# Performance work log

Measured on AMD Instinct MI355X. Metric: run time of the kernel, lower is better.

The kernel has to match this reference:

```python
import jax, jax.numpy as jnp
import numpy as np

EPS = 1e-06


def setup_inputs() -> dict:
    key = jax.random.key(0)
    k1, k2, k3 = jax.random.split(key, 3)
    B, L, S, C = 128, 512, 512, 64
    q = jax.random.normal(k1, (B, L, C), dtype=jnp.float32)
    k = jax.random.normal(k2, (B, S, C), dtype=jnp.float32)
    labels = jax.random.randint(k3, (B, L, S), 0, 2, dtype=jnp.int64)
    return {"q": q, "k": k, "labels": labels}


def reference(q, k, labels):
    # sim: [B, L, S], mapped to (0, 1) via (1 + cos-like sim) / 2
    sim = (1.0 + jnp.einsum('blc,bsc->bls', q, k)) * 0.5

    # column-wise stats (over L) -> [B, S]; torch.std uses ddof=1 (unbiased)
    col = (jnp.max(sim, axis=1) - jnp.mean(sim, axis=1)) / jnp.std(sim, axis=1, ddof=1)
    sharp1 = jax.nn.softmax(col, axis=-1)  # [B, S]

    # row-wise stats (over S) -> [B, L]
    row = (jnp.max(sim, axis=2) - jnp.mean(sim, axis=2)) / jnp.std(sim, axis=2, ddof=1)
    sharp2 = jax.nn.softmax(row, axis=-1)  # [B, L]

    simc = jnp.clip(sim, EPS, 1.0 - EPS)
    nll = -jnp.log(simc)                    # [B, L, S]
    nll_neg = -jnp.log(1.0 - simc)          # [B, L, S]

    pos = (labels == 1).astype(sim.dtype)
    neg = (labels == 0).astype(sim.dtype)

    # masked sums per sample, weighted by sharpness (broadcast over rows/cols)
    loss1 = jnp.sum(nll * sharp1[:, None, :] * pos, axis=(1, 2))  # [B]
    loss2 = jnp.sum(nll * sharp2[:, :, None] * pos, axis=(1, 2))  # [B]
    loss3 = jnp.sum(nll_neg * neg, axis=(1, 2)) / jnp.sum(neg, axis=(1, 2))  # [B]

    losses = (loss1 + loss2) * 0.5 + loss3
    return (sharp1, jnp.mean(losses))
```

## Files before the change

### kernel.cpp

```cpp
#include <hip/hip_runtime.h>

#define EPSF 1e-6f

typedef _Float16 half8 __attribute__((ext_vector_type(8)));
typedef float f32x4 __attribute__((ext_vector_type(4)));

constexpr int B = 128, L = 512, S = 512, C = 64;
constexpr int TILE_R = 64;
constexpr int TILES  = L / TILE_R;
constexpr int CHUNK  = 64;
constexpr int NCHUNK = S / CHUNK;
constexpr int HALVES = 2;
constexpr int CPB    = NCHUNK / HALVES;

constexpr size_t WS_COLMAX = 0;
constexpr size_t WS_COLSUM = WS_COLMAX + (size_t)B * TILES * S;
constexpr size_t WS_COLSSQ = WS_COLSUM + (size_t)B * TILES * S;
constexpr size_t WS_COLP1  = WS_COLSSQ + (size_t)B * TILES * S;
constexpr size_t WS_ROWMAX = WS_COLP1  + (size_t)B * TILES * S;
constexpr size_t WS_ROWSUM = WS_ROWMAX + (size_t)B * L * HALVES;
constexpr size_t WS_ROWSSQ = WS_ROWSUM + (size_t)B * L * HALVES;
constexpr size_t WS_ROWP2  = WS_ROWSSQ + (size_t)B * L * HALVES;
constexpr size_t WS_NEGS   = WS_ROWP2  + (size_t)B * L * HALVES;
constexpr size_t WS_NEGC   = WS_NEGS   + (size_t)B * TILES * HALVES;

__device__ inline void loadTile(const float* __restrict__ g, float4 v[4], int t)
{
    const float* src = g + (t >> 2) * 64 + (t & 3) * 16;
    v[0] = *(const float4*)(src);
    v[1] = *(const float4*)(src + 4);
    v[2] = *(const float4*)(src + 8);
    v[3] = *(const float4*)(src + 12);
}

__device__ inline void stageW(const float4 v4[4], half8 (*hiA)[64], half8 (*loA)[64], int t)
{
    const int row = t >> 2, c0 = (t & 3) * 16;
    const float v[16] = {v4[0].x, v4[0].y, v4[0].z, v4[0].w, v4[1].x, v4[1].y, v4[1].z, v4[1].w,
                         v4[2].x, v4[2].y, v4[2].z, v4[2].w, v4[3].x, v4[3].y, v4[3].z, v4[3].w};
#pragma unroll
    for (int o = 0; o < 2; ++o) {
        const int cb     = c0 + o * 8;
        const int idx    = (row >> 4) * 2 + (cb >> 5);
        const int lane_s = (((cb >> 3) & 3) << 4) + (row & 15);
        half8 h, l;
#pragma unroll
        for (int j = 0; j < 8; ++j) {
            float f = v[o * 8 + j];
            _Float16 hi = (_Float16)f;
            h[j] = hi;
            l[j] = (_Float16)(f - (float)hi);
        }
        hiA[idx][lane_s] = h;
        loA[idx][lane_s] = l;
    }
}

__global__ __launch_bounds__(256) __attribute__((amdgpu_waves_per_eu(3, 8)))
void pass1_kernel(const float* __restrict__ q, const float* __restrict__ kmat,
                  const int* __restrict__ labels, float* __restrict__ ws)
{
    __shared__ half8 khiF[8][64], kloF[8][64];
    __shared__ float4 colred4[4][CHUNK];
    __shared__ float nred[4][2];

    const int bidx = blockIdx.x;
    const int b    = bidx / (TILES * HALVES);
    const int rem  = bidx % (TILES * HALVES);
    const int tile = rem >> 1;
    const int half = rem & 1;
    const int chbase = half * CPB;
    const int tid  = threadIdx.x;
    const int lane = tid & 63;
    const int wave = tid >> 6;
    const int l15  = lane & 15;
    const int quad = lane >> 4;
    const int rowbase = tile * TILE_R;

    float* colmax_p = ws + WS_COLMAX;
    float* colsum_p = ws + WS_COLSUM;
    float* colssq_p = ws + WS_COLSSQ;
    float* colp1_p  = ws + WS_COLP1;
    float* rowmax_p = ws + WS_ROWMAX;
    float* rowsum_p = ws + WS_ROWSUM;
    float* rowssq_p = ws + WS_ROWSSQ;
    float* rowp2_p  = ws + WS_ROWP2;
    float* negs_p   = ws + WS_NEGS;
    float* negc_p   = ws + WS_NEGC;

    const float* kb = kmat + (size_t)b * S * C;
    const int*   lb = labels + ((size_t)b * L + rowbase) * S;

    float4 tv[4];
    loadTile(q + ((size_t)b * L + rowbase) * C, tv, tid);
    stageW(tv, khiF, kloF, tid);
    int labn[16];
#pragma unroll
    for (int ct = 0; ct < 4; ++ct)
#pragma unroll
        for (int r = 0; r < 4; ++r)
            labn[ct * 4 + r] = lb[(size_t)(wave * 16 + quad * 4 + r) * S
                                  + chbase * CHUNK + ct * 16 + l15];
    __syncthreads();
    half8 ah0 = khiF[wave * 2 + 0][lane], ah1 = khiF[wave * 2 + 1][lane];
    half8 al0 = kloF[wave * 2 + 0][lane], al1 = kloF[wave * 2 + 1][lane];
    loadTile(kb + (size_t)chbase * CHUNK * C, tv, tid);

    float rmax[4], rsum[4], rssq[4], rp2[4];
#pragma unroll
    for (int i = 0; i < 4; ++i) { rmax[i] = -3.4e38f; rsum[i] = 0.f; rssq[i] = 0.f; rp2[i] = 0.f; }
    float negsum = 0.f;
    int   possum = 0;

    for (int c4 = 0; c4 < CPB; ++c4) {
        const int ch = chbase + c4;
        __syncthreads();
        if (c4 > 0 && tid < CHUNK) {
            float4 v = colred4[0][tid];
            float m0 = v.x, s1 = v.y, s2 = v.z, pp = v.w;
#pragma unroll
            for (int w = 1; w < 4; ++w) {
                float4 u = colred4[w][tid];
                m0 = fmaxf(m0, u.x); s1 += u.y; s2 += u.z; pp += u.w;
            }
            size_t idx = ((size_t)b * TILES + tile) * S + (ch - 1) * CHUNK + tid;
            colmax_p[idx] = m0; colsum_p[idx] = s1; colssq_p[idx] = s2; colp1_p[idx] = pp;
        }
        stageW(tv, khiF, kloF, tid);
        if (c4 + 1 < CPB)
            loadTile(kb + (size_t)(ch + 1) * CHUNK * C, tv, tid);
        __syncthreads();

        f32x4 acc[4];
#pragma unroll
        for (int ct = 0; ct < 4; ++ct) {
            half8 bh0 = khiF[ct * 2 + 0][lane], bh1 = khiF[ct * 2 + 1][lane];
            half8 bl0 = kloF[ct * 2 + 0][lane], bl1 = kloF[ct * 2 + 1][lane];
            f32x4 a = {0.f, 0.f, 0.f, 0.f};
            a = __builtin_amdgcn_mfma_f32_16x16x32_f16(ah0, bh0, a, 0, 0, 0);
            a = __builtin_amdgcn_mfma_f32_16x16x32_f16(ah0, bl0, a, 0, 0, 0);
            a = __builtin_amdgcn_mfma_f32_16x16x32_f16(al0, bh0, a, 0, 0, 0);
            a = __builtin_amdgcn_mfma_f32_16x16x32_f16(ah1, bh1, a, 0, 0, 0);
            a = __builtin_amdgcn_mfma_f32_16x16x32_f16(ah1, bl1, a, 0, 0, 0);
            a = __builtin_amdgcn_mfma_f32_16x16x32_f16(al1, bh1, a, 0, 0, 0);
            acc[ct] = a;
        }

#pragma unroll
        for (int ct = 0; ct < 4; ++ct) {
            float cmax = -3.4e38f, csum = 0.f, cssq = 0.f, cp1 = 0.f;
#pragma unroll
            for (int r = 0; r < 4; ++r) {
                int lab = labn[ct * 4 + r];
                float sim = fmaf(0.5f, acc[ct][r], 0.5f);
                rmax[r] = fmaxf(rmax[r], sim);
                rsum[r] += sim;
                rssq[r] = fmaf(sim, sim, rssq[r]);
                cmax = fmaxf(cmax, sim);
                csum += sim;
                cssq = fmaf(sim, sim, cssq);
                float sc  = fminf(fmaxf(sim, EPSF), 1.f - EPSF);
                bool  isp = (lab == 1);
                float pos = isp ? 1.f : 0.f;
                float t   = isp ? sc : (1.f - sc);
                float nl  = -__logf(t);
                float pn  = pos * nl;
                rp2[r] += pn;
                cp1 += pn;
                negsum += nl - pn;
                possum += lab;
            }
#pragma unroll
            for (int m = 16; m <= 32; m <<= 1) {
                cmax = fmaxf(cmax, __shfl_xor(cmax, m, 64));
                csum += __shfl_xor(csum, m, 64);
                cssq += __shfl_xor(cssq, m, 64);
                cp1  += __shfl_xor(cp1,  m, 64);
            }
            if (lane < 16)
                colred4[wave][ct * 16 + l15] = make_float4(cmax, csum, cssq, cp1);
        }

        if (c4 + 1 < CPB) {
#pragma unroll
            for (int ct = 0; ct < 4; ++ct)
#pragma unroll
                for (int r = 0; r < 4; ++r)
                    labn[ct * 4 + r] = lb[(size_t)(wave * 16 + quad * 4 + r) * S
                                          + (ch + 1) * CHUNK + ct * 16 + l15];
        }
    }

    __syncthreads();
    if (tid < CHUNK) {
        float4 v = colred4[0][tid];
        float m0 = v.x, s1 = v.y, s2 = v.z, pp = v.w;
#pragma unroll
        for (int w = 1; w < 4; ++w) {
            float4 u = colred4[w][tid];
            m0 = fmaxf(m0, u.x); s1 += u.y; s2 += u.z; pp += u.w;
        }
        size_t idx = ((size_t)b * TILES + tile) * S + (chbase + CPB - 1) * CHUNK + tid;
        colmax_p[idx] = m0; colsum_p[idx] = s1; colssq_p[idx] = s2; colp1_p[idx] = pp;
    }

#pragma unroll
    for (int r = 0; r < 4; ++r) {
#pragma unroll
        for (int m = 1; m <= 8; m <<= 1) {
            rmax[r] = fmaxf(rmax[r], __shfl_xor(rmax[r], m, 64));
            rsum[r] += __shfl_xor(rsum[r], m, 64);
            rssq[r] += __shfl_xor(rssq[r], m, 64);
            rp2[r]  += __shfl_xor(rp2[r],  m, 64);
        }
    }
    if (l15 == 0) {
#pragma unroll
        for (int r = 0; r < 4; ++r) {
            size_t idx = ((size_t)b * L + rowbase + wave * 16 + quad * 4 + r) * HALVES + half;
            rowmax_p[idx] = rmax[r]; rowsum_p[idx] = rsum[r];
            rowssq_p[idx] = rssq[r]; rowp2_p[idx]  = rp2[r];
        }
    }

    float negcnt = (float)(16 * CPB - possum);
#pragma unroll
    for (int m = 1; m <= 32; m <<= 1) {
        negsum += __shfl_xor(negsum, m, 64);
        negcnt += __shfl_xor(negcnt, m, 64);
    }
    if (lane == 0) { nred[wave][0] = negsum; nred[wave][1] = negcnt; }
    __syncthreads();
    if (tid == 0) {
        float ns = 0.f, nc = 0.f;
        for (int w = 0; w < 4; ++w) { ns += nred[w][0]; nc += nred[w][1]; }
        negs_p[bidx] = ns; negc_p[bidx] = nc;
    }
}

template <bool MAX>
__device__ inline float bred(float v, float* red)
{
#pragma unroll
    for (int m = 1; m <= 32; m <<= 1) {
        float o = __shfl_xor(v, m, 64);
        v = MAX ? fmaxf(v, o) : (v + o);
    }
    const int wave = threadIdx.x >> 6;
    const int lane = threadIdx.x & 63;
    if (lane == 0) red[wave] = v;
    __syncthreads();
    if (threadIdx.x == 0) {
        float r = red[0];
        for (int w = 1; w < 8; ++w) r = MAX ? fmaxf(r, red[w]) : (r + red[w]);
        red[8] = r;
    }
    __syncthreads();
    float out = red[8];
    __syncthreads();
    return out;
}

__global__ __launch_bounds__(512)
void pass2_kernel(const float* __restrict__ ws, float* __restrict__ out)
{
    __shared__ float red[9];
    const int b = blockIdx.x;
    const int s = threadIdx.x;

    if (blockIdx.y == 0) {
        const float* colmax_p = ws + WS_COLMAX;
        const float* colsum_p = ws + WS_COLSUM;
        const float* colssq_p = ws + WS_COLSSQ;
        const float* colp1_p  = ws + WS_COLP1;

        float m = -3.4e38f, sm = 0.f, sq = 0.f, p1 = 0.f;
#pragma unroll
        for (int t = 0; t < TILES; ++t) {
            size_t idx = ((size_t)b * TILES + t) * S + s;
            m = fmaxf(m, colmax_p[idx]);
            sm += colsum_p[idx];
            sq += colssq_p[idx];
            p1 += colp1_p[idx];
        }
        float mean  = sm * (1.f / L);
        float var   = (sq - sm * sm * (1.f / L)) * (1.f / (L - 1));
        float score = (m - mean) / sqrtf(var);

        float gmax = bred<true>(score, red);
        float e    = __expf(score - gmax);
        float esum = bred<false>(e, red);
        float sharp1 = e / esum;
        out[(size_t)b * S + s] = sharp1;
        float loss1 = bred<false>(sharp1 * p1, red);
        if (s == 0) atomicAdd(out + (size_t)B * S, loss1 * (0.5f / B));
    } else {
        const float* rowmax_p = ws + WS_ROWMAX;
        const float* rowsum_p = ws + WS_ROWSUM;
        const float* rowssq_p = ws + WS_ROWSSQ;
        const float* rowp2_p  = ws + WS_ROWP2;
        const float* negs_p   = ws + WS_NEGS;
        const float* negc_p   = ws + WS_NEGC;

        size_t ridx = ((size_t)b * L + s) * HALVES;
        float m2 = rowmax_p[ridx], sm2 = rowsum_p[ridx];
        float sq2 = rowssq_p[ridx], p2 = rowp2_p[ridx];
#pragma unroll
        for (int h = 1; h < HALVES; ++h) {
            m2 = fmaxf(m2, rowmax_p[ridx + h]);
            sm2 += rowsum_p[ridx + h];
            sq2 += rowssq_p[ridx + h];
            p2  += rowp2_p[ridx + h];
        }
        float mean2  = sm2 * (1.f / S);
        float var2   = (sq2 - sm2 * sm2 * (1.f / S)) * (1.f / (S - 1));
        float score2 = (m2 - mean2) / sqrtf(var2);

        float gmax2 = bred<true>(score2, red);
        float e2    = __expf(score2 - gmax2);
        float esum2 = bred<false>(e2, red);
        float loss2 = bred<false>((e2 / esum2) * p2, red);

        if (s == 0) {
            float ns = 0.f, nc = 0.f;
            for (int t = 0; t < TILES * HALVES; ++t) {
                ns += negs_p[b * TILES * HALVES + t];
                nc += negc_p[b * TILES * HALVES + t];
            }
            atomicAdd(out + (size_t)B * S, (0.5f * loss2 + ns / nc) * (1.f / B));
        }
    }
}

extern "C" void kernel_launch(void* const* d_in, const int* in_sizes, int n_in,
                              void* d_out, int out_size, void* d_ws, size_t ws_size,
                              hipStream_t stream)
{
    const float* q      = (const float*)d_in[0];
    const float* k      = (const float*)d_in[1];
    const int*   labels = (const int*)d_in[2];
    float* out = (float*)d_out;
    float* ws  = (float*)d_ws;

    hipMemsetAsync((char*)d_out + (size_t)B * S * sizeof(float), 0, sizeof(float), stream);

    pass1_kernel<<<dim3(B * TILES * HALVES), dim3(256), 0, stream>>>(q, k, labels, ws);
    pass2_kernel<<<dim3(B, 2), dim3(512), 0, stream>>>(ws, out);
}
```

Baseline: 240.1 us.

## Precompute fp16 hi/lo MFMA fragments in a separate kernel, drop LDS staging

```diff
diff --git a/kernel.cpp b/kernel.cpp
--- a/kernel.cpp
+++ b/kernel.cpp
@@ -23,6 +23,8 @@
 constexpr size_t WS_ROWP2  = WS_ROWSSQ + (size_t)B * L * HALVES;
 constexpr size_t WS_NEGS   = WS_ROWP2  + (size_t)B * L * HALVES;
 constexpr size_t WS_NEGC   = WS_NEGS   + (size_t)B * TILES * HALVES;
+constexpr size_t WS_QF     = WS_NEGC   + (size_t)B * TILES * HALVES;
+constexpr size_t WS_KF     = WS_QF     + (size_t)B * TILES * 4096;
 
 __device__ inline void loadTile(const float* __restrict__ g, float4 v[4], int t)
 {
@@ -33,7 +35,7 @@
     v[3] = *(const float4*)(src + 12);
 }
 
-__device__ inline void stageW(const float4 v4[4], half8 (*hiA)[64], half8 (*loA)[64], int t)
+__device__ inline void fragStore(const float4 v4[4], half8* dhi, half8* dlo, int t)
 {
     const int row = t >> 2, c0 = (t & 3) * 16;
     const float v[16] = {v4[0].x, v4[0].y, v4[0].z, v4[0].w, v4[1].x, v4[1].y, v4[1].z, v4[1].w,
@@ -51,17 +53,35 @@
             h[j] = hi;
             l[j] = (_Float16)(f - (float)hi);
         }
-        hiA[idx][lane_s] = h;
-        loA[idx][lane_s] = l;
-    }
+        dhi[idx * 64 + lane_s] = h;
+        dlo[idx * 64 + lane_s] = l;
+    }
+}
+
+__global__ __launch_bounds__(256)
+void convert_kernel(const float* __restrict__ q, const float* __restrict__ kmat,
+                    float* __restrict__ ws)
+{
+    const int bidx = blockIdx.x;
+    const int b    = bidx >> 4;
+    const int t16  = bidx & 15;
+    const int tid  = threadIdx.x;
+    const bool isq = (t16 < TILES);
+    const int tile = isq ? t16 : t16 - TILES;
+
+    const float* src = isq ? (q    + ((size_t)b * L + (size_t)tile * TILE_R) * C)
+                           : (kmat + ((size_t)b * S + (size_t)tile * CHUNK)  * C);
+    half8* base = (half8*)(ws + (isq ? WS_QF : WS_KF)) + (size_t)(b * TILES + tile) * 1024;
+
+    float4 v[4];
+    loadTile(src, v, tid);
+    fragStore(v, base, base + 512, tid);
 }
 
 __global__ __launch_bounds__(256) __attribute__((amdgpu_waves_per_eu(3, 8)))
-void pass1_kernel(const float* __restrict__ q, const float* __restrict__ kmat,
-                  const int* __restrict__ labels, float* __restrict__ ws)
-{
-    __shared__ half8 khiF[8][64], kloF[8][64];
-    __shared__ float4 colred4[4][CHUNK];
+void pass1_kernel(const int* __restrict__ labels, float* __restrict__ ws)
+{
+    __shared__ float4 colred4[4][CPB][CHUNK];
     __shared__ float nred[4][2];
 
     const int bidx = blockIdx.x;
@@ -88,23 +108,23 @@
     float* negs_p   = ws + WS_NEGS;
     float* negc_p   = ws + WS_NEGC;
 
-    const float* kb = kmat + (size_t)b * S * C;
-    const int*   lb = labels + ((size_t)b * L + rowbase) * S;
-
-    float4 tv[4];
-    loadTile(q + ((size_t)b * L + rowbase) * C, tv, tid);
-    stageW(tv, khiF, kloF, tid);
+    const int* lb = labels + ((size_t)b * L + rowbase) * S;
+
+    const half8* qf  = (const half8*)(ws + WS_QF) + (size_t)(b * TILES + tile) * 1024;
+    const half8* kf0 = (const half8*)(ws + WS_KF) + (size_t)b * NCHUNK * 1024;
+
+    half8 ah0 = qf[(wave * 2 + 0) * 64 + lane];
+    half8 ah1 = qf[(wave * 2 + 1) * 64 + lane];
+    half8 al0 = qf[512 + (wave * 2 + 0) * 64 + lane];
+    half8 al1 = qf[512 + (wave * 2 + 1) * 64 + lane];
+
     int labn[16];
 #pragma unroll
     for (int ct = 0; ct < 4; ++ct)
 #pragma unroll
         for (int r = 0; r < 4; ++r)
-            labn[ct * 4 + r] = lb[(size_t)(wave * 16 + quad * 4 + r) * S
-                                  + chbase * CHUNK + ct * 16 + l15];
-    __syncthreads();
-    half8 ah0 = khiF[wave * 2 + 0][lane], ah1 = khiF[wave * 2 + 1][lane];
-    half8 al0 = kloF[wave * 2 + 0][lane], al1 = kloF[wave * 2 + 1][lane];
-    loadTile(kb + (size_t)chbase * CHUNK * C, tv, tid);
+            labn[ct * 4 + r] = __builtin_nontemporal_load(
+                &lb[(size_t)(wave * 16 + quad * 4 + r) * S + chbase * CHUNK + ct * 16 + l15]);
 
     float rmax[4], rsum[4], rssq[4], rp2[4];
 #pragma unroll
@@ -114,28 +134,15 @@
 
     for (int c4 = 0; c4 < CPB; ++c4) {
         const int ch = chbase + c4;
-        __syncthreads();
-        if (c4 > 0 && tid < CHUNK) {
-            float4 v = colred4[0][tid];
-            float m0 = v.x, s1 = v.y, s2 = v.z, pp = v.w;
-#pragma unroll
-            for (int w = 1; w < 4; ++w) {
-                float4 u = colred4[w][tid];
-                m0 = fmaxf(m0, u.x); s1 += u.y; s2 += u.z; pp += u.w;
-            }
-            size_t idx = ((size_t)b * TILES + tile) * S + (ch - 1) * CHUNK + tid;
-            colmax_p[idx] = m0; colsum_p[idx] = s1; colssq_p[idx] = s2; colp1_p[idx] = pp;
-        }
-        stageW(tv, khiF, kloF, tid);
-        if (c4 + 1 < CPB)
-            loadTile(kb + (size_t)(ch + 1) * CHUNK * C, tv, tid);
-        __syncthreads();
+        const half8* kfc = kf0 + (size_t)ch * 1024;
 
         f32x4 acc[4];
 #pragma unroll
         for (int ct = 0; ct < 4; ++ct) {
-            half8 bh0 = khiF[ct * 2 + 0][lane], bh1 = khiF[ct * 2 + 1][lane];
-            half8 bl0 = kloF[ct * 2 + 0][lane], bl1 = kloF[ct * 2 + 1][lane];
+            half8 bh0 = kfc[(ct * 2 + 0) * 64 + lane];
+            half8 bh1 = kfc[(ct * 2 + 1) * 64 + lane];
+            half8 bl0 = kfc[512 + (ct * 2 + 0) * 64 + lane];
+            half8 bl1 = kfc[512 + (ct * 2 + 1) * 64 + lane];
             f32x4 a = {0.f, 0.f, 0.f, 0.f};
             a = __builtin_amdgcn_mfma_f32_16x16x32_f16(ah0, bh0, a, 0, 0, 0);
             a = __builtin_amdgcn_mfma_f32_16x16x32_f16(ah0, bl0, a, 0, 0, 0);
@@ -178,7 +185,7 @@
                 cp1  += __shfl_xor(cp1,  m, 64);
             }
             if (lane < 16)
-                colred4[wave][ct * 16 + l15] = make_float4(cmax, csum, cssq, cp1);
+                colred4[wave][c4][ct * 16 + l15] = make_float4(cmax, csum, cssq, cp1);
         }
 
         if (c4 + 1 < CPB) {
@@ -186,21 +193,23 @@
             for (int ct = 0; ct < 4; ++ct)
 #pragma unroll
                 for (int r = 0; r < 4; ++r)
-                    labn[ct * 4 + r] = lb[(size_t)(wave * 16 + quad * 4 + r) * S
-                                          + (ch + 1) * CHUNK + ct * 16 + l15];
-        }
-    }
-
-    __syncthreads();
-    if (tid < CHUNK) {
-        float4 v = colred4[0][tid];
+                    labn[ct * 4 + r] = __builtin_nontemporal_load(
+                        &lb[(size_t)(wave * 16 + quad * 4 + r) * S + (ch + 1) * CHUNK + ct * 16 + l15]);
+        }
+    }
+
+    __syncthreads();
+    {
+        const int cc  = tid >> 6;
+        const int col = tid & 63;
+        float4 v = colred4[0][cc][col];
         float m0 = v.x, s1 = v.y, s2 = v.z, pp = v.w;
 #pragma unroll
         for (int w = 1; w < 4; ++w) {
-            float4 u = colred4[w][tid];
+            float4 u = colred4[w][cc][col];
             m0 = fmaxf(m0, u.x); s1 += u.y; s2 += u.z; pp += u.w;
         }
-        size_t idx = ((size_t)b * TILES + tile) * S + (chbase + CPB - 1) * CHUNK + tid;
+        size_t idx = ((size_t)b * TILES + tile) * S + (chbase + cc) * CHUNK + col;
         colmax_p[idx] = m0; colsum_p[idx] = s1; colssq_p[idx] = s2; colp1_p[idx] = pp;
     }
 
@@ -344,6 +353,7 @@
 
     hipMemsetAsync((char*)d_out + (size_t)B * S * sizeof(float), 0, sizeof(float), stream);
 
-    pass1_kernel<<<dim3(B * TILES * HALVES), dim3(256), 0, stream>>>(q, k, labels, ws);
+    convert_kernel<<<dim3(B * (TILES + NCHUNK)), dim3(256), 0, stream>>>(q, k, ws);
+    pass1_kernel<<<dim3(B * TILES * HALVES), dim3(256), 0, stream>>>(labels, ws);
     pass2_kernel<<<dim3(B, 2), dim3(512), 0, stream>>>(ws, out);
 }
```

Result: slower. 269.1 us (+12.0%).
